# Kernel optimization log

Measured on AMD Instinct MI355X. Metric: run time of the kernel, lower is better.

Reference implementation:

```python
import jax, jax.numpy as jnp
import numpy as np

B, N, D_IN, D_OUT, H = 262144, 6, 64, 64, 1
DH = D_OUT // H            # per-head feature dim
ALPHA = 0.2                # LeakyReLU negative slope
NEG = -9e15                # mask fill value from the original module


def setup_inputs() -> dict:
    key = jax.random.key(0)
    ks = jax.random.split(key, 9)
    s = 0.15  # ~xavier scale for 64x64
    node = jax.random.normal(ks[0], (B, N, D_IN), dtype=jnp.float32)
    adj = jax.random.randint(ks[1], (N, N), 0, 2, dtype=jnp.int32)
    W0 = jax.random.normal(ks[2], (D_OUT, D_IN), dtype=jnp.float32) * s
    b0 = jax.random.normal(ks[3], (D_OUT,), dtype=jnp.float32) * 0.01
    W1 = jax.random.normal(ks[4], (D_OUT, D_OUT), dtype=jnp.float32) * s
    b1 = jax.random.normal(ks[5], (D_OUT,), dtype=jnp.float32) * 0.01
    W2 = jax.random.normal(ks[6], (D_OUT, D_OUT), dtype=jnp.float32) * s
    b2 = jax.random.normal(ks[7], (D_OUT,), dtype=jnp.float32) * 0.01
    a = jax.random.normal(ks[8], (H, 2 * DH), dtype=jnp.float32) * s
    return {"node": node, "adj": adj, "W0": W0, "b0": b0,
            "W1": W1, "b1": b1, "W2": W2, "b2": b2, "a": a}


def reference(node, adj, W0, b0, W1, b1, W2, b2, a):
    # Three stacked linear projections (as in the original forward)
    x = node @ W0.T + b0          # [B, N, D_OUT]
    x = x @ W1.T + b1
    x = x @ W2.T + b2
    xh = x.reshape(B, N, H, DH)   # [B, N, H, DH]

    # Edge attention logit decomposes: a . [x_i || x_j] = a_src.x_i + a_dst.x_j.
    # Compute densely over the 6x6 node pairs instead of nonzero+gather+scatter;
    # identical math at kept positions, masked positions get -9e15 as original.
    a_src, a_dst = a[:, :DH], a[:, DH:]
    e_src = jnp.einsum('bnhc,hc->bnh', xh, a_src)  # [B, N, H]
    e_dst = jnp.einsum('bnhc,hc->bnh', xh, a_dst)  # [B, N, H]
    z = e_src[:, :, None, :] + e_dst[:, None, :, :]  # [B, i, j, H]
    logits = jnp.where(z >= 0, z, ALPHA * z)         # LeakyReLU(0.2)
    mask = (adj == 1)[None, :, :, None]              # same adj for every batch
    logits = jnp.where(mask, logits, NEG)
    probs = jax.nn.softmax(logits, axis=2)           # softmax over source j

    out = jnp.einsum('bijh,bjhc->bihc', probs, xh)   # aggregate neighbors
    return out.reshape(B, N, H * DH)                 # bConcat=True
```

## Files before the change

kernel.cpp:

```cpp
#include <hip/hip_runtime.h>
#include <stdint.h>

typedef short v8s __attribute__((ext_vector_type(8)));
typedef float v4f __attribute__((ext_vector_type(4)));
typedef uint16_t u16;

#define NB8   32768
#define ALPHA 0.2f
#define NEGV  -9000000000000000.0f

__device__ __forceinline__ uint32_t bf16rne(float f) {
    uint32_t u = __float_as_uint(f);
    return (u + 0x7FFFu + ((u >> 16) & 1u)) >> 16;
}
__device__ __forceinline__ uint32_t pk2(float lo, float hi) {
    return bf16rne(lo) | (bf16rne(hi) << 16);
}

__global__ __launch_bounds__(256) void gat_pre(
    const float* __restrict__ W0, const float* __restrict__ b0,
    const float* __restrict__ W1, const float* __restrict__ b1,
    const float* __restrict__ W2, const float* __restrict__ b2,
    float* __restrict__ bc_out, u16* __restrict__ wcb16)
{
    __shared__ float T[64 * 64];
    __shared__ float tb[64];
    const int t = threadIdx.x;
    for (int s = 0; s < 16; ++s) {
        int idx = t + 256 * s; int i = idx >> 6, j = idx & 63;
        float acc = 0.f;
        for (int k = 0; k < 64; ++k) acc = fmaf(W1[i * 64 + k], W0[k * 64 + j], acc);
        T[idx] = acc;
    }
    if (t < 64) {
        float acc = b1[t];
        for (int k = 0; k < 64; ++k) acc = fmaf(W1[t * 64 + k], b0[k], acc);
        tb[t] = acc;
    }
    __syncthreads();
    for (int s = 0; s < 16; ++s) {
        int idx = t + 256 * s; int i = idx >> 6, j = idx & 63;
        float acc = 0.f;
        for (int k = 0; k < 64; ++k) acc = fmaf(W2[i * 64 + k], T[k * 64 + j], acc);
        wcb16[idx] = (u16)bf16rne(acc);
    }
    if (t < 64) {
        float acc = b2[t];
        for (int k = 0; k < 64; ++k) acc = fmaf(W2[t * 64 + k], tb[k], acc);
        bc_out[t] = acc;
    }
}

__global__ __launch_bounds__(256, 2) void gat_main(
    const float* __restrict__ node, const int* __restrict__ adj,
    const float* __restrict__ a, const float* __restrict__ bc,
    const u16* __restrict__ wcb16, float* __restrict__ out)
{
    __shared__ u16      xtile[4][48 * 64];
    __shared__ float    ebuf2[4][2][48];
    __shared__ uint32_t pbuf[4][48][4];

    const int tid  = threadIdx.x;
    const int w    = tid >> 6;
    const int lane = tid & 63;
    const int a_   = lane & 15;
    const int h    = lane >> 4;

    uint64_t amask = 0ull;
    #pragma unroll 1
    for (int ij = 0; ij < 36; ++ij) amask |= ((uint64_t)(adj[ij] & 1)) << ij;

    v8s Bw[4][2];
    #pragma unroll
    for (int n = 0; n < 4; ++n)
        #pragma unroll
        for (int kt = 0; kt < 2; ++kt)
            Bw[n][kt] = *(const v8s*)(wcb16 + (16 * n + a_) * 64 + 32 * kt + 8 * h);
    float bcl[4], a_s[4], a_d[4];
    #pragma unroll
    for (int n = 0; n < 4; ++n) {
        bcl[n] = bc[16 * n + a_];
        a_s[n] = a[16 * n + a_];
        a_d[n] = a[64 + 16 * n + a_];
    }

    u16*   xt  = &xtile[w][0];
    float* ebs = &ebuf2[w][0][0];
    float* ebd = &ebuf2[w][1][0];

    const int nwaves = (int)((gridDim.x * blockDim.x) >> 6);
    const int wgid   = (int)((blockIdx.x * blockDim.x + tid) >> 6);

    float4 Araw[3][2][2];
    {
        const char* nb = (const char*)node + (size_t)wgid * 12288 + a_ * 256 + h * 32;
        #pragma unroll
        for (int t = 0; t < 3; ++t) {
            const char* bt = nb + t * 4096;
            Araw[t][0][0] = *(const float4*)(bt);
            Araw[t][0][1] = *(const float4*)(bt + 16);
            Araw[t][1][0] = *(const float4*)(bt + 128);
            Araw[t][1][1] = *(const float4*)(bt + 144);
        }
    }

    #pragma unroll 1
    for (int g = wgid; g < NB8; g += nwaves) {
        v8s A[3][2];
        #pragma unroll
        for (int t = 0; t < 3; ++t)
            #pragma unroll
            for (int kt = 0; kt < 2; ++kt) {
                union { uint32_t u[4]; v8s v; } f;
                f.u[0] = pk2(Araw[t][kt][0].x, Araw[t][kt][0].y);
                f.u[1] = pk2(Araw[t][kt][0].z, Araw[t][kt][0].w);
                f.u[2] = pk2(Araw[t][kt][1].x, Araw[t][kt][1].y);
                f.u[3] = pk2(Araw[t][kt][1].z, Araw[t][kt][1].w);
                A[t][kt] = f.v;
            }
        if (g + nwaves < NB8) {
            const char* nb = (const char*)node + (size_t)(g + nwaves) * 12288 + a_ * 256 + h * 32;
            #pragma unroll
            for (int t = 0; t < 3; ++t) {
                const char* bt = nb + t * 4096;
                Araw[t][0][0] = *(const float4*)(bt);
                Araw[t][0][1] = *(const float4*)(bt + 16);
                Araw[t][1][0] = *(const float4*)(bt + 128);
                Araw[t][1][1] = *(const float4*)(bt + 144);
            }
        }

        #pragma unroll
        for (int t = 0; t < 3; ++t) {
            float es_p[4] = { 0.f, 0.f, 0.f, 0.f };
            float ed_p[4] = { 0.f, 0.f, 0.f, 0.f };
            #pragma unroll
            for (int n = 0; n < 4; ++n) {
                v4f acc = { bcl[n], bcl[n], bcl[n], bcl[n] };
                acc = __builtin_amdgcn_mfma_f32_16x16x32_bf16(A[t][0], Bw[n][0], acc, 0, 0, 0);
                acc = __builtin_amdgcn_mfma_f32_16x16x32_bf16(A[t][1], Bw[n][1], acc, 0, 0, 0);
                uint32_t p01 = pk2(acc[0], acc[1]);
                uint32_t p23 = pk2(acc[2], acc[3]);
                const int cb = (16 * n + a_) ^ (h << 4);
                const int rb = (16 * t + 4 * h) * 64 + cb;
                xt[rb]       = (u16)p01;
                xt[rb + 64]  = (u16)(p01 >> 16);
                xt[rb + 128] = (u16)p23;
                xt[rb + 192] = (u16)(p23 >> 16);
                #pragma unroll
                for (int r = 0; r < 4; ++r) {
                    es_p[r] = fmaf(acc[r], a_s[n], es_p[r]);
                    ed_p[r] = fmaf(acc[r], a_d[n], ed_p[r]);
                }
            }
            #pragma unroll
            for (int r = 0; r < 4; ++r) {
                #pragma unroll
                for (int m = 8; m > 0; m >>= 1) {
                    es_p[r] += __shfl_xor(es_p[r], m, 16);
                    ed_p[r] += __shfl_xor(ed_p[r], m, 16);
                }
            }
            if (a_ == 0) {
                #pragma unroll
                for (int r = 0; r < 4; ++r) ebs[16 * t + 4 * h + r] = es_p[r];
            }
            if (a_ == 1) {
                #pragma unroll
                for (int r = 0; r < 4; ++r) ebd[16 * t + 4 * h + r] = ed_p[r];
            }
        }
        asm volatile("s_waitcnt lgkmcnt(0)" ::: "memory");
        __builtin_amdgcn_sched_barrier(0);

        if (lane < 48) {
            const int bb = lane / 6;
            const int i6 = lane - 6 * bb;
            float es = ebs[lane];
            float ed[6];
            #pragma unroll
            for (int k = 0; k < 3; ++k)
                *(float2*)&ed[2 * k] = *(const float2*)(ebd + 6 * bb + 2 * k);
            uint32_t rm = (uint32_t)((amask >> (i6 * 6)) & 63u);
            float l[6];
            #pragma unroll
            for (int j = 0; j < 6; ++j) {
                float z  = es + ed[j];
                float lk = fmaxf(z, ALPHA * z);
                l[j] = (rm & (1u << j)) ? lk : NEGV;
            }
            float mm = fmaxf(fmaxf(fmaxf(l[0], l[1]), fmaxf(l[2], l[3])), fmaxf(l[4], l[5]));
            float p[6]; float sum = 0.f;
            #pragma unroll
            for (int j = 0; j < 6; ++j) { p[j] = __expf(l[j] - mm); sum += p[j]; }
            float inv = 1.0f / sum;
            uint4 pk;
            pk.x = pk2(p[0] * inv, p[1] * inv);
            pk.y = pk2(p[2] * inv, p[3] * inv);
            pk.z = pk2(p[4] * inv, p[5] * inv);
            pk.w = 0u;
            *(uint4*)&pbuf[w][lane][0] = pk;
        }
        asm volatile("s_waitcnt lgkmcnt(0)" ::: "memory");
        __builtin_amdgcn_sched_barrier(0);

        #pragma unroll 2
        for (int bb = 0; bb < 8; ++bb) {
            float xr[6];
            #pragma unroll
            for (int jj = 0; jj < 6; ++jj) {
                int rj = 6 * bb + jj;
                u16 xv = xt[rj * 64 + (lane ^ ((((rj >> 2) & 3)) << 4))];
                xr[jj] = __uint_as_float(((uint32_t)xv) << 16);
            }
            float* dst = out + ((size_t)(g * 8 + bb)) * 384 + lane;
            #pragma unroll
            for (int i2 = 0; i2 < 6; ++i2) {
                uint4 pu = *(const uint4*)&pbuf[w][bb * 6 + i2][0];
                float p0 = __uint_as_float(pu.x << 16);
                float p1 = __uint_as_float(pu.x & 0xFFFF0000u);
                float p2 = __uint_as_float(pu.y << 16);
                float p3 = __uint_as_float(pu.y & 0xFFFF0000u);
                float p4 = __uint_as_float(pu.z << 16);
                float p5 = __uint_as_float(pu.z & 0xFFFF0000u);
                float o = p0 * xr[0];
                o = fmaf(p1, xr[1], o);
                o = fmaf(p2, xr[2], o);
                o = fmaf(p3, xr[3], o);
                o = fmaf(p4, xr[4], o);
                o = fmaf(p5, xr[5], o);
                dst[i2 * 64] = o;
            }
        }
        asm volatile("s_waitcnt lgkmcnt(0)" ::: "memory");
        __builtin_amdgcn_sched_barrier(0);
    }
}

extern "C" void kernel_launch(void* const* d_in, const int* in_sizes, int n_in,
                              void* d_out, int out_size, void* d_ws, size_t ws_size,
                              hipStream_t stream)
{
    const float* node = (const float*)d_in[0];
    const int*   adj  = (const int*)d_in[1];
    const float* W0   = (const float*)d_in[2];
    const float* b0   = (const float*)d_in[3];
    const float* W1   = (const float*)d_in[4];
    const float* b1   = (const float*)d_in[5];
    const float* W2   = (const float*)d_in[6];
    const float* b2   = (const float*)d_in[7];
    const float* a    = (const float*)d_in[8];
    float* outp = (float*)d_out;

    float* wsf   = (float*)d_ws;
    float* bcp   = wsf;
    u16*   wcb16 = (u16*)(wsf + 64);

    gat_pre<<<1, 256, 0, stream>>>(W0, b0, W1, b1, W2, b2, bcp, wcb16);
    gat_main<<<1024, 256, 0, stream>>>(node, adj, a, bcp, wcb16, outp);
}
```

Measured before the change: 207.9 us.

## Shrink per-wave tile to 2 batches, stage weights in LDS, raise occupancy

Each wave now handles 2 batch elements (12 rows, padded to 16 for the MFMA) per iteration instead of 8 (48 rows). This cuts register and LDS use so launch bounds can target 8 blocks per CU. The combined weight matrix moves from per-lane registers into swizzled LDS and is reloaded for every MFMA. The grid doubles to 2048 blocks. The aim is to hide memory latency through higher occupancy, at the cost of 4 of 16 MFMA rows doing wasted work, extra LDS reads, and more loop overhead per byte.

```diff
diff --git a/kernel.cpp b/kernel.cpp
--- a/kernel.cpp
+++ b/kernel.cpp
@@ -5,7 +5,7 @@
 typedef float v4f __attribute__((ext_vector_type(4)));
 typedef uint16_t u16;
 
-#define NB8   32768
+#define NB2   131072
 #define ALPHA 0.2f
 #define NEGV  -9000000000000000.0f
 
@@ -51,14 +51,16 @@
     }
 }
 
-__global__ __launch_bounds__(256, 2) void gat_main(
+__global__ __launch_bounds__(256, 8) void gat_main(
     const float* __restrict__ node, const int* __restrict__ adj,
     const float* __restrict__ a, const float* __restrict__ bc,
     const u16* __restrict__ wcb16, float* __restrict__ out)
 {
-    __shared__ u16      xtile[4][48 * 64];
-    __shared__ float    ebuf2[4][2][48];
-    __shared__ uint32_t pbuf[4][48][4];
+    __shared__ u16      wc_lds[64 * 64];
+    __shared__ float    a_sh[128];
+    __shared__ u16      xtile[4][16 * 64];
+    __shared__ float    ebuf2[4][2][12];
+    __shared__ uint32_t pbuf[4][12][4];
 
     const int tid  = threadIdx.x;
     const int w    = tid >> 6;
@@ -66,22 +68,28 @@
     const int a_   = lane & 15;
     const int h    = lane >> 4;
 
+    {
+        #pragma unroll
+        for (int m = 0; m < 2; ++m) {
+            int flat = tid * 2 + m;
+            int r = flat >> 3, p = flat & 7;
+            uint4 v = *(const uint4*)((const char*)wcb16 + flat * 16);
+            *(uint4*)((char*)wc_lds + (size_t)(r * 8 + (p ^ (r & 7))) * 16) = v;
+        }
+        if (tid < 128) a_sh[tid] = a[tid];
+    }
+    __syncthreads();
+
     uint64_t amask = 0ull;
     #pragma unroll 1
     for (int ij = 0; ij < 36; ++ij) amask |= ((uint64_t)(adj[ij] & 1)) << ij;
 
-    v8s Bw[4][2];
-    #pragma unroll
-    for (int n = 0; n < 4; ++n)
-        #pragma unroll
-        for (int kt = 0; kt < 2; ++kt)
-            Bw[n][kt] = *(const v8s*)(wcb16 + (16 * n + a_) * 64 + 32 * kt + 8 * h);
     float bcl[4], a_s[4], a_d[4];
     #pragma unroll
     for (int n = 0; n < 4; ++n) {
         bcl[n] = bc[16 * n + a_];
-        a_s[n] = a[16 * n + a_];
-        a_d[n] = a[64 + 16 * n + a_];
+        a_s[n] = a_sh[16 * n + a_];
+        a_d[n] = a_sh[64 + 16 * n + a_];
     }
 
     u16*   xt  = &xtile[w][0];
@@ -91,89 +99,85 @@
     const int nwaves = (int)((gridDim.x * blockDim.x) >> 6);
     const int wgid   = (int)((blockIdx.x * blockDim.x + tid) >> 6);
 
-    float4 Araw[3][2][2];
+    const int rowoff = (a_ < 12 ? a_ : 0) * 256;
+
+    float4 Araw[4];
     {
-        const char* nb = (const char*)node + (size_t)wgid * 12288 + a_ * 256 + h * 32;
-        #pragma unroll
-        for (int t = 0; t < 3; ++t) {
-            const char* bt = nb + t * 4096;
-            Araw[t][0][0] = *(const float4*)(bt);
-            Araw[t][0][1] = *(const float4*)(bt + 16);
-            Araw[t][1][0] = *(const float4*)(bt + 128);
-            Araw[t][1][1] = *(const float4*)(bt + 144);
-        }
+        const char* nb = (const char*)node + (size_t)wgid * 3072 + rowoff + h * 32;
+        Araw[0] = *(const float4*)(nb);
+        Araw[1] = *(const float4*)(nb + 16);
+        Araw[2] = *(const float4*)(nb + 128);
+        Araw[3] = *(const float4*)(nb + 144);
     }
 
     #pragma unroll 1
-    for (int g = wgid; g < NB8; g += nwaves) {
-        v8s A[3][2];
-        #pragma unroll
-        for (int t = 0; t < 3; ++t)
-            #pragma unroll
-            for (int kt = 0; kt < 2; ++kt) {
-                union { uint32_t u[4]; v8s v; } f;
-                f.u[0] = pk2(Araw[t][kt][0].x, Araw[t][kt][0].y);
-                f.u[1] = pk2(Araw[t][kt][0].z, Araw[t][kt][0].w);
-                f.u[2] = pk2(Araw[t][kt][1].x, Araw[t][kt][1].y);
-                f.u[3] = pk2(Araw[t][kt][1].z, Araw[t][kt][1].w);
-                A[t][kt] = f.v;
-            }
-        if (g + nwaves < NB8) {
-            const char* nb = (const char*)node + (size_t)(g + nwaves) * 12288 + a_ * 256 + h * 32;
-            #pragma unroll
-            for (int t = 0; t < 3; ++t) {
-                const char* bt = nb + t * 4096;
-                Araw[t][0][0] = *(const float4*)(bt);
-                Araw[t][0][1] = *(const float4*)(bt + 16);
-                Araw[t][1][0] = *(const float4*)(bt + 128);
-                Araw[t][1][1] = *(const float4*)(bt + 144);
-            }
-        }
-
-        #pragma unroll
-        for (int t = 0; t < 3; ++t) {
-            float es_p[4] = { 0.f, 0.f, 0.f, 0.f };
-            float ed_p[4] = { 0.f, 0.f, 0.f, 0.f };
-            #pragma unroll
-            for (int n = 0; n < 4; ++n) {
-                v4f acc = { bcl[n], bcl[n], bcl[n], bcl[n] };
-                acc = __builtin_amdgcn_mfma_f32_16x16x32_bf16(A[t][0], Bw[n][0], acc, 0, 0, 0);
-                acc = __builtin_amdgcn_mfma_f32_16x16x32_bf16(A[t][1], Bw[n][1], acc, 0, 0, 0);
-                uint32_t p01 = pk2(acc[0], acc[1]);
-                uint32_t p23 = pk2(acc[2], acc[3]);
-                const int cb = (16 * n + a_) ^ (h << 4);
-                const int rb = (16 * t + 4 * h) * 64 + cb;
-                xt[rb]       = (u16)p01;
-                xt[rb + 64]  = (u16)(p01 >> 16);
-                xt[rb + 128] = (u16)p23;
-                xt[rb + 192] = (u16)(p23 >> 16);
-                #pragma unroll
-                for (int r = 0; r < 4; ++r) {
-                    es_p[r] = fmaf(acc[r], a_s[n], es_p[r]);
-                    ed_p[r] = fmaf(acc[r], a_d[n], ed_p[r]);
-                }
-            }
+    for (int g = wgid; g < NB2; g += nwaves) {
+        v8s A0, A1;
+        {
+            union { uint32_t u[4]; v8s v; } f;
+            f.u[0] = pk2(Araw[0].x, Araw[0].y);
+            f.u[1] = pk2(Araw[0].z, Araw[0].w);
+            f.u[2] = pk2(Araw[1].x, Araw[1].y);
+            f.u[3] = pk2(Araw[1].z, Araw[1].w);
+            A0 = f.v;
+            f.u[0] = pk2(Araw[2].x, Araw[2].y);
+            f.u[1] = pk2(Araw[2].z, Araw[2].w);
+            f.u[2] = pk2(Araw[3].x, Araw[3].y);
+            f.u[3] = pk2(Araw[3].z, Araw[3].w);
+            A1 = f.v;
+        }
+        if (g + nwaves < NB2) {
+            const char* nb = (const char*)node + (size_t)(g + nwaves) * 3072 + rowoff + h * 32;
+            Araw[0] = *(const float4*)(nb);
+            Araw[1] = *(const float4*)(nb + 16);
+            Araw[2] = *(const float4*)(nb + 128);
+            Araw[3] = *(const float4*)(nb + 144);
+        }
+
+        float es_p[4] = { 0.f, 0.f, 0.f, 0.f };
+        float ed_p[4] = { 0.f, 0.f, 0.f, 0.f };
+        #pragma unroll
+        for (int n = 0; n < 4; ++n) {
+            const char* wrow = (const char*)wc_lds + (16 * n + a_) * 128;
+            v8s b0 = *(const v8s*)(wrow + (((h    ) ^ (a_ & 7)) << 4));
+            v8s b1 = *(const v8s*)(wrow + (((4 + h) ^ (a_ & 7)) << 4));
+            v4f acc = { bcl[n], bcl[n], bcl[n], bcl[n] };
+            acc = __builtin_amdgcn_mfma_f32_16x16x32_bf16(A0, b0, acc, 0, 0, 0);
+            acc = __builtin_amdgcn_mfma_f32_16x16x32_bf16(A1, b1, acc, 0, 0, 0);
+            uint32_t p01 = pk2(acc[0], acc[1]);
+            uint32_t p23 = pk2(acc[2], acc[3]);
+            const int cb = (16 * n + a_) ^ (h << 4);
+            const int rb = (4 * h) * 64 + cb;
+            xt[rb]       = (u16)p01;
+            xt[rb + 64]  = (u16)(p01 >> 16);
+            xt[rb + 128] = (u16)p23;
+            xt[rb + 192] = (u16)(p23 >> 16);
             #pragma unroll
             for (int r = 0; r < 4; ++r) {
-                #pragma unroll
-                for (int m = 8; m > 0; m >>= 1) {
-                    es_p[r] += __shfl_xor(es_p[r], m, 16);
-                    ed_p[r] += __shfl_xor(ed_p[r], m, 16);
-                }
-            }
-            if (a_ == 0) {
-                #pragma unroll
-                for (int r = 0; r < 4; ++r) ebs[16 * t + 4 * h + r] = es_p[r];
-            }
-            if (a_ == 1) {
-                #pragma unroll
-                for (int r = 0; r < 4; ++r) ebd[16 * t + 4 * h + r] = ed_p[r];
-            }
+                es_p[r] = fmaf(acc[r], a_s[n], es_p[r]);
+                ed_p[r] = fmaf(acc[r], a_d[n], ed_p[r]);
+            }
+        }
+        #pragma unroll
+        for (int r = 0; r < 4; ++r) {
+            #pragma unroll
+            for (int m = 8; m > 0; m >>= 1) {
+                es_p[r] += __shfl_xor(es_p[r], m, 16);
+                ed_p[r] += __shfl_xor(ed_p[r], m, 16);
+            }
+        }
+        if (a_ == 0) {
+            #pragma unroll
+            for (int r = 0; r < 4; ++r) { int row = 4 * h + r; if (row < 12) ebs[row] = es_p[r]; }
+        }
+        if (a_ == 1) {
+            #pragma unroll
+            for (int r = 0; r < 4; ++r) { int row = 4 * h + r; if (row < 12) ebd[row] = ed_p[r]; }
         }
         asm volatile("s_waitcnt lgkmcnt(0)" ::: "memory");
         __builtin_amdgcn_sched_barrier(0);
 
-        if (lane < 48) {
+        if (lane < 12) {
             const int bb = lane / 6;
             const int i6 = lane - 6 * bb;
             float es = ebs[lane];
@@ -204,8 +208,8 @@
         asm volatile("s_waitcnt lgkmcnt(0)" ::: "memory");
         __builtin_amdgcn_sched_barrier(0);
 
-        #pragma unroll 2
-        for (int bb = 0; bb < 8; ++bb) {
+        #pragma unroll
+        for (int bb = 0; bb < 2; ++bb) {
             float xr[6];
             #pragma unroll
             for (int jj = 0; jj < 6; ++jj) {
@@ -213,7 +217,7 @@
                 u16 xv = xt[rj * 64 + (lane ^ ((((rj >> 2) & 3)) << 4))];
                 xr[jj] = __uint_as_float(((uint32_t)xv) << 16);
             }
-            float* dst = out + ((size_t)(g * 8 + bb)) * 384 + lane;
+            float* dst = out + ((size_t)(g * 2 + bb)) * 384 + lane;
             #pragma unroll
             for (int i2 = 0; i2 < 6; ++i2) {
                 uint4 pu = *(const uint4*)&pbuf[w][bb * 6 + i2][0];
@@ -257,5 +261,5 @@
     u16*   wcb16 = (u16*)(wsf + 64);
 
     gat_pre<<<1, 256, 0, stream>>>(W0, b0, W1, b1, W2, b2, bcp, wcb16);
-    gat_main<<<1024, 256, 0, stream>>>(node, adj, a, bcp, wcb16, outp);
-}
+    gat_main<<<2048, 256, 0, stream>>>(node, adj, a, bcp, wcb16, outp);
+}
```

After: 410.6 us. +97.4%, slower.

## Stage input and output through swizzled LDS for coalesced 16-byte nontemporal global access

Applied to the files above, without the earlier changes.

Input rows are now loaded as fully contiguous 16-byte-per-lane nontemporal loads, converted to bf16, and written into an XOR-swizzled LDS tile from which MFMA A-fragments are read. The output aggregation now computes 4 columns per lane and stages results in a swizzled LDS buffer, then writes them with coalesced 16-byte nontemporal stores. The explicit lgkmcnt waits and scheduling barriers are removed, and launch bounds are raised to 3 blocks per CU. This adds LDS traffic and footprint, and dropping the explicit waits relies on the compiler to order the wave-private LDS accesses correctly.

```diff
diff --git a/kernel.cpp b/kernel.cpp
--- a/kernel.cpp
+++ b/kernel.cpp
@@ -51,12 +51,13 @@
     }
 }
 
-__global__ __launch_bounds__(256, 2) void gat_main(
+__global__ __launch_bounds__(256, 3) void gat_main(
     const float* __restrict__ node, const int* __restrict__ adj,
     const float* __restrict__ a, const float* __restrict__ bc,
     const u16* __restrict__ wcb16, float* __restrict__ out)
 {
-    __shared__ u16      xtile[4][48 * 64];
+    __shared__ __align__(16) u16      bufX[4][3072];
+    __shared__ __align__(16) float    bufO[4][1536];
     __shared__ float    ebuf2[4][2][48];
     __shared__ uint32_t pbuf[4][48][4];
 
@@ -84,51 +85,47 @@
         a_d[n] = a[64 + 16 * n + a_];
     }
 
-    u16*   xt  = &xtile[w][0];
+    char*  xs  = (char*)&bufX[w][0];
+    char*  osf = (char*)&bufO[w][0];
     float* ebs = &ebuf2[w][0][0];
     float* ebd = &ebuf2[w][1][0];
 
     const int nwaves = (int)((gridDim.x * blockDim.x) >> 6);
     const int wgid   = (int)((blockIdx.x * blockDim.x + tid) >> 6);
 
-    float4 Araw[3][2][2];
+    v4f Araw[12];
     {
-        const char* nb = (const char*)node + (size_t)wgid * 12288 + a_ * 256 + h * 32;
-        #pragma unroll
-        for (int t = 0; t < 3; ++t) {
-            const char* bt = nb + t * 4096;
-            Araw[t][0][0] = *(const float4*)(bt);
-            Araw[t][0][1] = *(const float4*)(bt + 16);
-            Araw[t][1][0] = *(const float4*)(bt + 128);
-            Araw[t][1][1] = *(const float4*)(bt + 144);
-        }
+        const float* nb = node + (size_t)wgid * 3072;
+        #pragma unroll
+        for (int m = 0; m < 12; ++m)
+            Araw[m] = __builtin_nontemporal_load((const v4f*)(nb + m * 256 + 4 * lane));
     }
 
     #pragma unroll 1
     for (int g = wgid; g < NB8; g += nwaves) {
+        #pragma unroll
+        for (int m = 0; m < 12; ++m) {
+            uint32_t lo = pk2(Araw[m][0], Araw[m][1]);
+            uint32_t hi = pk2(Araw[m][2], Araw[m][3]);
+            int r    = 4 * m + (lane >> 4);
+            int byte = r * 128 + (((((lane & 15) >> 1)) ^ (r & 7)) << 4) + ((lane & 1) << 3);
+            uint2 v; v.x = lo; v.y = hi;
+            *(uint2*)(xs + byte) = v;
+        }
+        if (g + nwaves < NB8) {
+            const float* nb = node + (size_t)(g + nwaves) * 3072;
+            #pragma unroll
+            for (int m = 0; m < 12; ++m)
+                Araw[m] = __builtin_nontemporal_load((const v4f*)(nb + m * 256 + 4 * lane));
+        }
         v8s A[3][2];
         #pragma unroll
         for (int t = 0; t < 3; ++t)
             #pragma unroll
             for (int kt = 0; kt < 2; ++kt) {
-                union { uint32_t u[4]; v8s v; } f;
-                f.u[0] = pk2(Araw[t][kt][0].x, Araw[t][kt][0].y);
-                f.u[1] = pk2(Araw[t][kt][0].z, Araw[t][kt][0].w);
-                f.u[2] = pk2(Araw[t][kt][1].x, Araw[t][kt][1].y);
-                f.u[3] = pk2(Araw[t][kt][1].z, Araw[t][kt][1].w);
-                A[t][kt] = f.v;
-            }
-        if (g + nwaves < NB8) {
-            const char* nb = (const char*)node + (size_t)(g + nwaves) * 12288 + a_ * 256 + h * 32;
-            #pragma unroll
-            for (int t = 0; t < 3; ++t) {
-                const char* bt = nb + t * 4096;
-                Araw[t][0][0] = *(const float4*)(bt);
-                Araw[t][0][1] = *(const float4*)(bt + 16);
-                Araw[t][1][0] = *(const float4*)(bt + 128);
-                Araw[t][1][1] = *(const float4*)(bt + 144);
-            }
-        }
+                int row = 16 * t + a_;
+                A[t][kt] = *(const v8s*)(xs + row * 128 + (((4 * kt + h) ^ (a_ & 7)) << 4));
+            }
 
         #pragma unroll
         for (int t = 0; t < 3; ++t) {
@@ -141,12 +138,15 @@
                 acc = __builtin_amdgcn_mfma_f32_16x16x32_bf16(A[t][1], Bw[n][1], acc, 0, 0, 0);
                 uint32_t p01 = pk2(acc[0], acc[1]);
                 uint32_t p23 = pk2(acc[2], acc[3]);
-                const int cb = (16 * n + a_) ^ (h << 4);
-                const int rb = (16 * t + 4 * h) * 64 + cb;
-                xt[rb]       = (u16)p01;
-                xt[rb + 64]  = (u16)(p01 >> 16);
-                xt[rb + 128] = (u16)p23;
-                xt[rb + 192] = (u16)(p23 >> 16);
+                const int colc = 2 * n + (a_ >> 3);
+                const int cin  = (a_ & 7) << 1;
+                u16 vs0 = (u16)p01, vs1 = (u16)(p01 >> 16);
+                u16 vs2 = (u16)p23, vs3 = (u16)(p23 >> 16);
+                int row0 = 16 * t + 4 * h;
+                *(u16*)(xs + (row0    ) * 128 + ((colc ^ ((row0    ) & 7)) << 4) + cin) = vs0;
+                *(u16*)(xs + (row0 + 1) * 128 + ((colc ^ ((row0 + 1) & 7)) << 4) + cin) = vs1;
+                *(u16*)(xs + (row0 + 2) * 128 + ((colc ^ ((row0 + 2) & 7)) << 4) + cin) = vs2;
+                *(u16*)(xs + (row0 + 3) * 128 + ((colc ^ ((row0 + 3) & 7)) << 4) + cin) = vs3;
                 #pragma unroll
                 for (int r = 0; r < 4; ++r) {
                     es_p[r] = fmaf(acc[r], a_s[n], es_p[r]);
@@ -170,8 +170,6 @@
                 for (int r = 0; r < 4; ++r) ebd[16 * t + 4 * h + r] = ed_p[r];
             }
         }
-        asm volatile("s_waitcnt lgkmcnt(0)" ::: "memory");
-        __builtin_amdgcn_sched_barrier(0);
 
         if (lane < 48) {
             const int bb = lane / 6;
@@ -201,39 +199,59 @@
             pk.w = 0u;
             *(uint4*)&pbuf[w][lane][0] = pk;
         }
-        asm volatile("s_waitcnt lgkmcnt(0)" ::: "memory");
-        __builtin_amdgcn_sched_barrier(0);
-
-        #pragma unroll 2
-        for (int bb = 0; bb < 8; ++bb) {
-            float xr[6];
-            #pragma unroll
-            for (int jj = 0; jj < 6; ++jj) {
-                int rj = 6 * bb + jj;
-                u16 xv = xt[rj * 64 + (lane ^ ((((rj >> 2) & 3)) << 4))];
-                xr[jj] = __uint_as_float(((uint32_t)xv) << 16);
-            }
-            float* dst = out + ((size_t)(g * 8 + bb)) * 384 + lane;
+
+        float* ob = out + (size_t)g * 3072;
+        #pragma unroll
+        for (int h2 = 0; h2 < 2; ++h2) {
+            const int b2 = lane >> 4;
+            const int q  = lane & 15;
+            const int B8 = 4 * h2 + b2;
+            uint2 xd[6];
+            #pragma unroll
+            for (int j = 0; j < 6; ++j) {
+                int rj = 6 * B8 + j;
+                xd[j] = *(const uint2*)(xs + rj * 128 + ((((q >> 1)) ^ (rj & 7)) << 4) + ((q & 1) << 3));
+            }
+            float xr[6][4];
+            #pragma unroll
+            for (int j = 0; j < 6; ++j) {
+                xr[j][0] = __uint_as_float(xd[j].x << 16);
+                xr[j][1] = __uint_as_float(xd[j].x & 0xFFFF0000u);
+                xr[j][2] = __uint_as_float(xd[j].y << 16);
+                xr[j][3] = __uint_as_float(xd[j].y & 0xFFFF0000u);
+            }
             #pragma unroll
             for (int i2 = 0; i2 < 6; ++i2) {
-                uint4 pu = *(const uint4*)&pbuf[w][bb * 6 + i2][0];
+                uint4 pu = *(const uint4*)&pbuf[w][6 * B8 + i2][0];
                 float p0 = __uint_as_float(pu.x << 16);
                 float p1 = __uint_as_float(pu.x & 0xFFFF0000u);
                 float p2 = __uint_as_float(pu.y << 16);
                 float p3 = __uint_as_float(pu.y & 0xFFFF0000u);
                 float p4 = __uint_as_float(pu.z << 16);
                 float p5 = __uint_as_float(pu.z & 0xFFFF0000u);
-                float o = p0 * xr[0];
-                o = fmaf(p1, xr[1], o);
-                o = fmaf(p2, xr[2], o);
-                o = fmaf(p3, xr[3], o);
-                o = fmaf(p4, xr[4], o);
-                o = fmaf(p5, xr[5], o);
-                dst[i2 * 64] = o;
-            }
-        }
-        asm volatile("s_waitcnt lgkmcnt(0)" ::: "memory");
-        __builtin_amdgcn_sched_barrier(0);
+                v4f o;
+                #pragma unroll
+                for (int c = 0; c < 4; ++c) {
+                    float acc0 = p0 * xr[0][c];
+                    acc0 = fmaf(p1, xr[1][c], acc0);
+                    acc0 = fmaf(p2, xr[2][c], acc0);
+                    acc0 = fmaf(p3, xr[3][c], acc0);
+                    acc0 = fmaf(p4, xr[4][c], acc0);
+                    acc0 = fmaf(p5, xr[5][c], acc0);
+                    o[c] = acc0;
+                }
+                int lr = 6 * b2 + i2;
+                int pc = q ^ ((lr & 3) << 2);
+                *(v4f*)(osf + lr * 256 + (pc << 4)) = o;
+            }
+            #pragma unroll
+            for (int m2 = 0; m2 < 6; ++m2) {
+                int rr  = 4 * m2 + (lane >> 4);
+                int pc2 = (lane & 15) ^ ((lane >> 4) << 2);
+                v4f v = *(const v4f*)(osf + rr * 256 + (pc2 << 4));
+                __builtin_nontemporal_store(v, (v4f*)(ob + h2 * 1536 + m2 * 256 + 4 * lane));
+            }
+        }
     }
 }
 
```

New measurement: 445.1 us. 2.14x slower.
